# Kernel tuning notes

Hardware: AMD Instinct MI355X
Metric: run time of the kernel (lower is better)

The kernel has to match this reference:

```python
import jax, jax.numpy as jnp
import numpy as np

DIM_MSA = 256
DIM_PAIR = 128
DIM_HID = 32
EPS = 0.001
LN_EPS = 1e-5


def setup_inputs() -> dict:
    key = jax.random.key(0)
    ks = jax.random.split(key, 8)
    b, m, n = 1, 256, 384
    x = jax.random.normal(ks[0], (b, m, n, DIM_MSA), dtype=jnp.float32)
    mask = jax.random.randint(ks[1], (b, m, n), 0, 2).astype(jnp.int32)
    ln_g = jnp.ones((DIM_MSA,), jnp.float32)
    ln_b = jnp.zeros((DIM_MSA,), jnp.float32)
    s = 1.0 / np.sqrt(DIM_MSA)
    wl = jax.random.normal(ks[2], (DIM_MSA, DIM_HID), jnp.float32) * s
    bl = jnp.zeros((DIM_HID,), jnp.float32)
    wr = jax.random.normal(ks[3], (DIM_MSA, DIM_HID), jnp.float32) * s
    br = jnp.zeros((DIM_HID,), jnp.float32)
    wo = jax.random.normal(ks[4], (DIM_HID * DIM_HID, DIM_PAIR), jnp.float32) / np.sqrt(DIM_HID * DIM_HID)
    bo = jnp.zeros((DIM_PAIR,), jnp.float32)
    return {"x": x, "mask": mask, "ln_g": ln_g, "ln_b": ln_b,
            "wl": wl, "bl": bl, "wr": wr, "br": br, "wo": wo, "bo": bo}


def reference(x, mask, ln_g, ln_b, wl, bl, wr, br, wo, bo):
    # LayerNorm over last dim
    mu = jnp.mean(x, axis=-1, keepdims=True)
    var = jnp.mean(jnp.square(x - mu), axis=-1, keepdims=True)
    xn = (x - mu) * jax.lax.rsqrt(var + LN_EPS) * ln_g + ln_b
    left = xn @ wl + bl    # [b,m,n,c]
    right = xn @ wr + br   # [b,m,n,d]
    m = mask.astype(x.dtype)  # 0/1 mask [b,m,n]
    left = left * m[..., None]
    right = right * m[..., None]
    # masked outer-product sum over MSA dim m, no 6D materialization
    outer = jnp.einsum('bmic,bmjd->bijcd', left, right)
    b_, i_, j_ = outer.shape[0], outer.shape[1], outer.shape[2]
    outer = outer.reshape(b_, i_, j_, DIM_HID * DIM_HID)
    out = outer @ wo + bo  # [b,i,j,pairwise]
    cnt = jnp.einsum('bmi,bmj->bij', m, m)  # valid-pair counts
    return out / (cnt[..., None] + EPS)
```

## Files before the change

### kernel.cpp

```cpp
#include <hip/hip_runtime.h>
#include <hip/hip_bf16.h>
#include <stdint.h>


typedef float f32x4 __attribute__((ext_vector_type(4)));
typedef __bf16 bf16x8 __attribute__((ext_vector_type(8)));

#define NSEQ 384
#define NMSA 256

typedef const __attribute__((address_space(1))) unsigned int* gptr_t;
typedef __attribute__((address_space(3))) unsigned int* lptr_t;

__device__ __forceinline__ void gload_lds16(const void* g, void* l) {
    __builtin_amdgcn_global_load_lds((gptr_t)g, (lptr_t)l, 16, 0, 0);
}

__global__ __launch_bounds__(256) void prep_kernel(
    const float* __restrict__ wl, const float* __restrict__ wr,
    const float* __restrict__ bl, const float* __restrict__ br,
    const float* __restrict__ wo,
    __bf16* __restrict__ woT, __bf16* __restrict__ wT, float* __restrict__ bias2)
{
    int gid = blockIdx.x * 256 + threadIdx.x;
    if (gid < 131072) {
        int p = gid >> 10, k = gid & 1023;
        woT[gid] = (__bf16)wo[k * 128 + p];
    } else if (gid < 131072 + 16384) {
        int r = gid - 131072;
        int c = r >> 8, k = r & 255;
        wT[r] = (__bf16)(c < 32 ? wl[k * 32 + c] : wr[k * 32 + (c - 32)]);
    } else if (gid < 131072 + 16384 + 64) {
        int c = gid - 147456;
        bias2[c] = (c < 32) ? bl[c] : br[c - 32];
    }
}

__global__ __launch_bounds__(256) void cnt_kernel(
    const int* __restrict__ mask, float* __restrict__ inv_cnt)
{
    const int i = blockIdx.x;
    const int t = threadIdx.x;
    __shared__ int mi[NMSA];
    mi[t] = mask[t * NSEQ + i];
    __syncthreads();
    for (int j = t; j < NSEQ; j += 256) {
        int acc = 0;
        for (int m = 0; m < NMSA; ++m)
            acc += mi[m] & mask[m * NSEQ + j];
        inv_cnt[i * NSEQ + j] = 1.0f / ((float)acc + 0.001f);
    }
}

__global__ __launch_bounds__(256) void ln_proj_kernel(
    const float* __restrict__ x, const int* __restrict__ mask,
    const float* __restrict__ ln_g, const float* __restrict__ ln_b,
    const __bf16* __restrict__ wT, const float* __restrict__ bias2,
    __bf16* __restrict__ leftT, __bf16* __restrict__ rightT)
{
    const int n = blockIdx.x;
    const int tid = threadIdx.x;
    __shared__ float muS[NMSA], rsS[NMSA], maskS[NMSA];
    __shared__ __bf16 xnT[NMSA * 40];

    {
        const float* xr = x + ((size_t)tid * NSEQ + n) * 256;
        float s = 0.f, sq = 0.f;
        for (int k = 0; k < 256; k += 4) {
            f32x4 v = *reinterpret_cast<const f32x4*>(xr + k);
            s  += v[0] + v[1] + v[2] + v[3];
            sq += v[0]*v[0] + v[1]*v[1] + v[2]*v[2] + v[3]*v[3];
        }
        float mu = s * (1.f / 256.f);
        float var = sq * (1.f / 256.f) - mu * mu;
        muS[tid] = mu;
        rsS[tid] = rsqrtf(var + 1e-5f);
        maskS[tid] = (float)mask[tid * NSEQ + n];
    }
    __syncthreads();

    const int wid = tid >> 6, lane = tid & 63;
    const int lhi = lane >> 4, llo = lane & 15;
    f32x4 acc[4][4] = {};

    for (int k0 = 0; k0 < 256; k0 += 32) {
        #pragma unroll
        for (int cc = 0; cc < 8; ++cc) {
            int ch = tid + cc * 256;
            int mR = ch >> 3, c4 = ch & 7;
            f32x4 v  = *reinterpret_cast<const f32x4*>(x + ((size_t)mR * NSEQ + n) * 256 + k0 + c4 * 4);
            f32x4 g  = *reinterpret_cast<const f32x4*>(ln_g + k0 + c4 * 4);
            f32x4 bb = *reinterpret_cast<const f32x4*>(ln_b + k0 + c4 * 4);
            float mu = muS[mR], rs = rsS[mR];
            __bf16* dst = xnT + mR * 40 + c4 * 4;
            dst[0] = (__bf16)((v[0] - mu) * rs * g[0] + bb[0]);
            dst[1] = (__bf16)((v[1] - mu) * rs * g[1] + bb[1]);
            dst[2] = (__bf16)((v[2] - mu) * rs * g[2] + bb[2]);
            dst[3] = (__bf16)((v[3] - mu) * rs * g[3] + bb[3]);
        }
        __syncthreads();
        bf16x8 af[4], bfr[4];
        #pragma unroll
        for (int fr = 0; fr < 4; ++fr)
            af[fr] = *reinterpret_cast<const bf16x8*>(wT + (size_t)(fr * 16 + llo) * 256 + k0 + lhi * 8);
        #pragma unroll
        for (int fc = 0; fc < 4; ++fc)
            bfr[fc] = *reinterpret_cast<const bf16x8*>(xnT + (wid * 64 + fc * 16 + llo) * 40 + lhi * 8);
        #pragma unroll
        for (int fr = 0; fr < 4; ++fr)
            #pragma unroll
            for (int fc = 0; fc < 4; ++fc)
                acc[fr][fc] = __builtin_amdgcn_mfma_f32_16x16x32_bf16(af[fr], bfr[fc], acc[fr][fc], 0, 0, 0);
        __syncthreads();
    }

    #pragma unroll
    for (int fr = 0; fr < 4; ++fr) {
        #pragma unroll
        for (int fc = 0; fc < 4; ++fc) {
            int mR = wid * 64 + fc * 16 + llo;
            float mv = maskS[mR];
            #pragma unroll
            for (int r = 0; r < 4; ++r) {
                int c = fr * 16 + lhi * 4 + r;
                __bf16 bv = (__bf16)((acc[fr][fc][r] + bias2[c]) * mv);
                if (c < 32) leftT [(size_t)(n * 32 + c)        * 256 + mR] = bv;
                else        rightT[(size_t)(n * 32 + (c - 32)) * 256 + mR] = bv;
            }
        }
    }
}

__global__ __launch_bounds__(512, 2) void outer_gemm_kernel(
    const __bf16* __restrict__ leftT, const __bf16* __restrict__ rightT,
    const __bf16* __restrict__ woT, const float* __restrict__ bo,
    const float* __restrict__ inv_cnt, float* __restrict__ out)
{
    __shared__ char smem[131072];
    const int tid = threadIdx.x;
    const int wid = tid >> 6, lane = tid & 63;
    const int lhi = lane >> 4, llo = lane & 15;
    const int wr = wid >> 2, wc = wid & 3;

    int wg = blockIdx.x;
    int l  = (wg & 7) * 288 + (wg >> 3);
    int bj = l / 48, bi = l % 48;

    char* Abuf[2] = { smem,         smem + 65536 };
    char* Bbuf[2] = { smem + 32768, smem + 98304 };

    auto STAGE = [&](int buf, int k0) {
        #pragma unroll
        for (int it = 0; it < 4; ++it) {
            int q = it * 512 + wid * 64 + lane;
            int r = q >> 3;
            int s = (q & 7) ^ (r & 7);
            int ldsoff = (it * 512 + wid * 64) * 16;
            gload_lds16(leftT  + (size_t)(bi * 256 + r) * 256 + k0 + s * 8, Abuf[buf] + ldsoff);
            gload_lds16(rightT + (size_t)(bj * 256 + r) * 256 + k0 + s * 8, Bbuf[buf] + ldsoff);
        }
    };

    f32x4 acc[8][4] = {};

    STAGE(0, 0);
    #pragma unroll
    for (int t = 0; t < 4; ++t) {
        if (t < 3) {
            STAGE((t + 1) & 1, (t + 1) * 64);
            asm volatile("s_waitcnt vmcnt(8)" ::: "memory");
        } else {
            asm volatile("s_waitcnt vmcnt(0)" ::: "memory");
        }
        __builtin_amdgcn_s_barrier();
        __builtin_amdgcn_sched_barrier(0);
        const __bf16* Al = (const __bf16*)Abuf[t & 1];
        const __bf16* Bl = (const __bf16*)Bbuf[t & 1];
        #pragma unroll
        for (int kk = 0; kk < 2; ++kk) {
            bf16x8 af[8], bfv[4];
            int sb = kk * 4 + lhi;
            #pragma unroll
            for (int fr = 0; fr < 8; ++fr) {
                int row = wr * 128 + fr * 16 + llo;
                af[fr] = *(const bf16x8*)(Al + row * 64 + ((sb ^ (row & 7)) << 3));
            }
            #pragma unroll
            for (int fc = 0; fc < 4; ++fc) {
                int row = wc * 64 + fc * 16 + llo;
                bfv[fc] = *(const bf16x8*)(Bl + row * 64 + ((sb ^ (row & 7)) << 3));
            }
            #pragma unroll
            for (int fr = 0; fr < 8; ++fr)
                #pragma unroll
                for (int fc = 0; fc < 4; ++fc)
                    acc[fr][fc] = __builtin_amdgcn_mfma_f32_16x16x32_bf16(af[fr], bfv[fc], acc[fr][fc], 0, 0, 0);
        }
        __builtin_amdgcn_sched_barrier(0);
        __builtin_amdgcn_s_barrier();
    }

    __bf16* Aep = (__bf16*)smem;
    #pragma unroll
    for (int fr = 0; fr < 8; ++fr) {
        #pragma unroll
        for (int fc = 0; fc < 4; ++fc) {
            int gj = wc * 64 + fc * 16 + llo;
            int jl = gj >> 5, d = gj & 31;
            #pragma unroll
            for (int r = 0; r < 4; ++r) {
                int gi = wr * 128 + fr * 16 + lhi * 4 + r;
                int il = gi >> 5, c = gi & 31;
                int ij = il * 8 + jl;
                int cd = c * 32 + d;
                int s = cd >> 3;
                int ss = s ^ ((s >> 4) & 7) ^ (ij & 7);
                Aep[ij * 1024 + (ss << 3) + (cd & 7)] = (__bf16)acc[fr][fc][r];
            }
        }
    }
    __builtin_amdgcn_s_barrier();
    __builtin_amdgcn_sched_barrier(0);

    f32x4 eacc[4] = {};
    const int p = wid * 16 + llo;
    const __bf16* wrow = woT + (size_t)p * 1024 + lhi * 8;
    #pragma unroll 4
    for (int k0 = 0; k0 < 1024; k0 += 32) {
        int sb = (k0 >> 3) + lhi;
        bf16x8 bw = *(const bf16x8*)(wrow + k0);
        #pragma unroll
        for (int mf = 0; mf < 4; ++mf) {
            int ij = mf * 16 + llo;
            int ss = sb ^ ((sb >> 4) & 7) ^ (ij & 7);
            bf16x8 a = *(const bf16x8*)(Aep + ij * 1024 + (ss << 3));
            eacc[mf] = __builtin_amdgcn_mfma_f32_16x16x32_bf16(a, bw, eacc[mf], 0, 0, 0);
        }
    }

    const float bov = bo[p];
    #pragma unroll
    for (int mf = 0; mf < 4; ++mf) {
        #pragma unroll
        for (int r = 0; r < 4; ++r) {
            int ij = mf * 16 + lhi * 4 + r;
            int i = bi * 8 + (ij >> 3);
            int j = bj * 8 + (ij & 7);
            size_t idx = (size_t)i * NSEQ + j;
            out[idx * 128 + p] = (eacc[mf][r] + bov) * inv_cnt[idx];
        }
    }
}

extern "C" void kernel_launch(void* const* d_in, const int* in_sizes, int n_in,
                              void* d_out, int out_size, void* d_ws, size_t ws_size,
                              hipStream_t stream) {
    const float* x    = (const float*)d_in[0];
    const int*   mask = (const int*)  d_in[1];
    const float* ln_g = (const float*)d_in[2];
    const float* ln_b = (const float*)d_in[3];
    const float* wl   = (const float*)d_in[4];
    const float* bl   = (const float*)d_in[5];
    const float* wr   = (const float*)d_in[6];
    const float* br   = (const float*)d_in[7];
    const float* wo   = (const float*)d_in[8];
    const float* bo   = (const float*)d_in[9];
    float* out = (float*)d_out;

    char* ws = (char*)d_ws;
    __bf16* leftT   = (__bf16*)(ws);
    __bf16* rightT  = (__bf16*)(ws + 6291456);
    __bf16* woT     = (__bf16*)(ws + 12582912);
    __bf16* wT      = (__bf16*)(ws + 12845056);
    float*  bias2   = (float*) (ws + 12877824);
    float*  inv_cnt = (float*) (ws + 12878080);

    prep_kernel<<<577, 256, 0, stream>>>(wl, wr, bl, br, wo, woT, wT, bias2);
    cnt_kernel<<<NSEQ, 256, 0, stream>>>(mask, inv_cnt);
    ln_proj_kernel<<<NSEQ, 256, 0, stream>>>(x, mask, ln_g, ln_b, wT, bias2, leftT, rightT);
    outer_gemm_kernel<<<2304, 512, 0, stream>>>(leftT, rightT, woT, bo, inv_cnt, out);
}
```

Measured before the change: 220.1 us.

## Fold LayerNorm into projection weights and split epilogue K across waves

LayerNorm gamma/beta are folded into the projection weights, with per-column sums precomputed. The projection kernel therefore reads x once, feeding raw bf16 x to the MFMA while accumulating row statistics, and applies mean/rstd correction in the epilogue. This removes the separate pass over x for statistics. In the outer GEMM epilogue, the accumulator write-out uses vectorized bf16x4 stores with a permuted woT layout, and the 1024-long K reduction is split across two wave groups combined through LDS. Rounding raw x to bf16 before subtracting the mean may cost some accuracy.

```diff
diff --git a/kernel.cpp b/kernel.cpp
--- a/kernel.cpp
+++ b/kernel.cpp
@@ -5,6 +5,7 @@
 
 typedef float f32x4 __attribute__((ext_vector_type(4)));
 typedef __bf16 bf16x8 __attribute__((ext_vector_type(8)));
+typedef __bf16 bf16x4 __attribute__((ext_vector_type(4)));
 
 #define NSEQ 384
 #define NMSA 256
@@ -17,22 +18,38 @@
 }
 
 __global__ __launch_bounds__(256) void prep_kernel(
+    const float* __restrict__ wo, __bf16* __restrict__ woT)
+{
+    int gid = blockIdx.x * 256 + threadIdx.x;
+    int p = gid >> 10, q = gid & 1023;
+    int d = q >> 5, c = q & 31;
+    woT[gid] = (__bf16)wo[(c * 32 + d) * 128 + p];
+}
+
+__global__ __launch_bounds__(256) void prep_wg_kernel(
     const float* __restrict__ wl, const float* __restrict__ wr,
     const float* __restrict__ bl, const float* __restrict__ br,
-    const float* __restrict__ wo,
-    __bf16* __restrict__ woT, __bf16* __restrict__ wT, float* __restrict__ bias2)
-{
-    int gid = blockIdx.x * 256 + threadIdx.x;
-    if (gid < 131072) {
-        int p = gid >> 10, k = gid & 1023;
-        woT[gid] = (__bf16)wo[k * 128 + p];
-    } else if (gid < 131072 + 16384) {
-        int r = gid - 131072;
-        int c = r >> 8, k = r & 255;
-        wT[r] = (__bf16)(c < 32 ? wl[k * 32 + c] : wr[k * 32 + (c - 32)]);
-    } else if (gid < 131072 + 16384 + 64) {
-        int c = gid - 147456;
-        bias2[c] = (c < 32) ? bl[c] : br[c - 32];
+    const float* __restrict__ ln_g, const float* __restrict__ ln_b,
+    __bf16* __restrict__ wg, float* __restrict__ Gc, float* __restrict__ B2)
+{
+    const int c = blockIdx.x;
+    const int k = threadIdx.x;
+    float w = (c < 32) ? wl[k * 32 + c] : wr[k * 32 + (c - 32)];
+    __bf16 wgb = (__bf16)(w * ln_g[k]);
+    wg[c * 256 + k] = wgb;
+    float gsum = (float)wgb;
+    float bsum = w * ln_b[k];
+    __shared__ float sg[4], sb[4];
+    for (int off = 32; off; off >>= 1) {
+        gsum += __shfl_down(gsum, off);
+        bsum += __shfl_down(bsum, off);
+    }
+    int wid = k >> 6, lane = k & 63;
+    if (lane == 0) { sg[wid] = gsum; sb[wid] = bsum; }
+    __syncthreads();
+    if (k == 0) {
+        Gc[c] = sg[0] + sg[1] + sg[2] + sg[3];
+        B2[c] = sb[0] + sb[1] + sb[2] + sb[3] + ((c < 32) ? bl[c] : br[c - 32]);
     }
 }
 
@@ -54,33 +71,21 @@
 
 __global__ __launch_bounds__(256) void ln_proj_kernel(
     const float* __restrict__ x, const int* __restrict__ mask,
-    const float* __restrict__ ln_g, const float* __restrict__ ln_b,
-    const __bf16* __restrict__ wT, const float* __restrict__ bias2,
+    const __bf16* __restrict__ wg, const float* __restrict__ Gc,
+    const float* __restrict__ B2,
     __bf16* __restrict__ leftT, __bf16* __restrict__ rightT)
 {
     const int n = blockIdx.x;
     const int tid = threadIdx.x;
-    __shared__ float muS[NMSA], rsS[NMSA], maskS[NMSA];
     __shared__ __bf16 xnT[NMSA * 40];
-
-    {
-        const float* xr = x + ((size_t)tid * NSEQ + n) * 256;
-        float s = 0.f, sq = 0.f;
-        for (int k = 0; k < 256; k += 4) {
-            f32x4 v = *reinterpret_cast<const f32x4*>(xr + k);
-            s  += v[0] + v[1] + v[2] + v[3];
-            sq += v[0]*v[0] + v[1]*v[1] + v[2]*v[2] + v[3]*v[3];
-        }
-        float mu = s * (1.f / 256.f);
-        float var = sq * (1.f / 256.f) - mu * mu;
-        muS[tid] = mu;
-        rsS[tid] = rsqrtf(var + 1e-5f);
-        maskS[tid] = (float)mask[tid * NSEQ + n];
-    }
-    __syncthreads();
+    __shared__ float muS[NMSA], rsS[NMSA], maskS[NMSA], GcS[64], B2S[64];
+
+    if (tid < 64) { GcS[tid] = Gc[tid]; B2S[tid] = B2[tid]; }
+    maskS[tid] = (float)mask[tid * NSEQ + n];
 
     const int wid = tid >> 6, lane = tid & 63;
     const int lhi = lane >> 4, llo = lane & 15;
+    float ps[8] = {}, pq[8] = {};
     f32x4 acc[4][4] = {};
 
     for (int k0 = 0; k0 < 256; k0 += 32) {
@@ -88,21 +93,18 @@
         for (int cc = 0; cc < 8; ++cc) {
             int ch = tid + cc * 256;
             int mR = ch >> 3, c4 = ch & 7;
-            f32x4 v  = *reinterpret_cast<const f32x4*>(x + ((size_t)mR * NSEQ + n) * 256 + k0 + c4 * 4);
-            f32x4 g  = *reinterpret_cast<const f32x4*>(ln_g + k0 + c4 * 4);
-            f32x4 bb = *reinterpret_cast<const f32x4*>(ln_b + k0 + c4 * 4);
-            float mu = muS[mR], rs = rsS[mR];
+            f32x4 v = *reinterpret_cast<const f32x4*>(x + ((size_t)mR * NSEQ + n) * 256 + k0 + c4 * 4);
+            ps[cc] += v[0] + v[1] + v[2] + v[3];
+            pq[cc] += v[0]*v[0] + v[1]*v[1] + v[2]*v[2] + v[3]*v[3];
             __bf16* dst = xnT + mR * 40 + c4 * 4;
-            dst[0] = (__bf16)((v[0] - mu) * rs * g[0] + bb[0]);
-            dst[1] = (__bf16)((v[1] - mu) * rs * g[1] + bb[1]);
-            dst[2] = (__bf16)((v[2] - mu) * rs * g[2] + bb[2]);
-            dst[3] = (__bf16)((v[3] - mu) * rs * g[3] + bb[3]);
+            dst[0] = (__bf16)v[0]; dst[1] = (__bf16)v[1];
+            dst[2] = (__bf16)v[2]; dst[3] = (__bf16)v[3];
         }
         __syncthreads();
         bf16x8 af[4], bfr[4];
         #pragma unroll
         for (int fr = 0; fr < 4; ++fr)
-            af[fr] = *reinterpret_cast<const bf16x8*>(wT + (size_t)(fr * 16 + llo) * 256 + k0 + lhi * 8);
+            af[fr] = *reinterpret_cast<const bf16x8*>(wg + (size_t)(fr * 16 + llo) * 256 + k0 + lhi * 8);
         #pragma unroll
         for (int fc = 0; fc < 4; ++fc)
             bfr[fc] = *reinterpret_cast<const bf16x8*>(xnT + (wid * 64 + fc * 16 + llo) * 40 + lhi * 8);
@@ -115,15 +117,32 @@
     }
 
     #pragma unroll
+    for (int cc = 0; cc < 8; ++cc) {
+        float s = ps[cc], q = pq[cc];
+        s += __shfl_xor(s, 1); q += __shfl_xor(q, 1);
+        s += __shfl_xor(s, 2); q += __shfl_xor(q, 2);
+        s += __shfl_xor(s, 4); q += __shfl_xor(q, 4);
+        if ((tid & 7) == 0) {
+            int m = (tid >> 3) + cc * 32;
+            float mu = s * (1.f / 256.f);
+            float var = q * (1.f / 256.f) - mu * mu;
+            muS[m] = mu;
+            rsS[m] = rsqrtf(var + 1e-5f);
+        }
+    }
+    __syncthreads();
+
+    #pragma unroll
     for (int fr = 0; fr < 4; ++fr) {
         #pragma unroll
         for (int fc = 0; fc < 4; ++fc) {
             int mR = wid * 64 + fc * 16 + llo;
-            float mv = maskS[mR];
+            float mv = maskS[mR], rs = rsS[mR], mu = muS[mR];
             #pragma unroll
             for (int r = 0; r < 4; ++r) {
                 int c = fr * 16 + lhi * 4 + r;
-                __bf16 bv = (__bf16)((acc[fr][fc][r] + bias2[c]) * mv);
+                float val = (acc[fr][fc][r] - mu * GcS[c]) * rs + B2S[c];
+                __bf16 bv = (__bf16)(val * mv);
                 if (c < 32) leftT [(size_t)(n * 32 + c)        * 256 + mR] = bv;
                 else        rightT[(size_t)(n * 32 + (c - 32)) * 256 + mR] = bv;
             }
@@ -142,8 +161,8 @@
     const int lhi = lane >> 4, llo = lane & 15;
     const int wr = wid >> 2, wc = wid & 3;
 
-    int wg = blockIdx.x;
-    int l  = (wg & 7) * 288 + (wg >> 3);
+    int wg_ = blockIdx.x;
+    int l  = (wg_ & 7) * 288 + (wg_ >> 3);
     int bj = l / 48, bi = l % 48;
 
     char* Abuf[2] = { smem,         smem + 65536 };
@@ -205,50 +224,66 @@
     for (int fr = 0; fr < 8; ++fr) {
         #pragma unroll
         for (int fc = 0; fc < 4; ++fc) {
-            int gj = wc * 64 + fc * 16 + llo;
-            int jl = gj >> 5, d = gj & 31;
-            #pragma unroll
-            for (int r = 0; r < 4; ++r) {
-                int gi = wr * 128 + fr * 16 + lhi * 4 + r;
-                int il = gi >> 5, c = gi & 31;
-                int ij = il * 8 + jl;
-                int cd = c * 32 + d;
-                int s = cd >> 3;
-                int ss = s ^ ((s >> 4) & 7) ^ (ij & 7);
-                Aep[ij * 1024 + (ss << 3) + (cd & 7)] = (__bf16)acc[fr][fc][r];
-            }
-        }
-    }
-    __builtin_amdgcn_s_barrier();
-    __builtin_amdgcn_sched_barrier(0);
-
-    f32x4 eacc[4] = {};
-    const int p = wid * 16 + llo;
-    const __bf16* wrow = woT + (size_t)p * 1024 + lhi * 8;
-    #pragma unroll 4
-    for (int k0 = 0; k0 < 1024; k0 += 32) {
-        int sb = (k0 >> 3) + lhi;
-        bf16x8 bw = *(const bf16x8*)(wrow + k0);
+            int ij = (wr * 4 + (fr >> 1)) * 8 + wc * 2 + (fc >> 1);
+            int half = fc & 1;
+            int t = llo * 4 + (fr & 1) * 2 + (lhi >> 1);
+            int tp = t ^ ((t >> 3) & 7) ^ (ij & 7);
+            bf16x4 v;
+            v[0] = (__bf16)acc[fr][fc][0]; v[1] = (__bf16)acc[fr][fc][1];
+            v[2] = (__bf16)acc[fr][fc][2]; v[3] = (__bf16)acc[fr][fc][3];
+            *(bf16x4*)(Aep + half * 32768 + ij * 512 + tp * 8 + (lhi & 1) * 4) = v;
+        }
+    }
+    __syncthreads();
+
+    const int kw = wid & 1, nw = wid >> 1;
+    const __bf16* Asrc = Aep + kw * 32768;
+    f32x4 eacc[4][2] = {};
+    #pragma unroll 2
+    for (int k0 = 0; k0 < 512; k0 += 32) {
+        bf16x8 bw0 = *(const bf16x8*)(woT + (size_t)(nw * 32 + llo)      * 1024 + kw * 512 + k0 + lhi * 8);
+        bf16x8 bw1 = *(const bf16x8*)(woT + (size_t)(nw * 32 + 16 + llo) * 1024 + kw * 512 + k0 + lhi * 8);
+        int t = (k0 >> 3) + lhi;
+        int txor = (t >> 3) & 7;
         #pragma unroll
         for (int mf = 0; mf < 4; ++mf) {
             int ij = mf * 16 + llo;
-            int ss = sb ^ ((sb >> 4) & 7) ^ (ij & 7);
-            bf16x8 a = *(const bf16x8*)(Aep + ij * 1024 + (ss << 3));
-            eacc[mf] = __builtin_amdgcn_mfma_f32_16x16x32_bf16(a, bw, eacc[mf], 0, 0, 0);
-        }
-    }
-
-    const float bov = bo[p];
-    #pragma unroll
-    for (int mf = 0; mf < 4; ++mf) {
-        #pragma unroll
-        for (int r = 0; r < 4; ++r) {
-            int ij = mf * 16 + lhi * 4 + r;
-            int i = bi * 8 + (ij >> 3);
-            int j = bj * 8 + (ij & 7);
-            size_t idx = (size_t)i * NSEQ + j;
-            out[idx * 128 + p] = (eacc[mf][r] + bov) * inv_cnt[idx];
-        }
+            int tp = t ^ txor ^ (ij & 7);
+            bf16x8 a = *(const bf16x8*)(Asrc + ij * 512 + tp * 8);
+            eacc[mf][0] = __builtin_amdgcn_mfma_f32_16x16x32_bf16(a, bw0, eacc[mf][0], 0, 0, 0);
+            eacc[mf][1] = __builtin_amdgcn_mfma_f32_16x16x32_bf16(a, bw1, eacc[mf][1], 0, 0, 0);
+        }
+    }
+    __syncthreads();
+
+    float* scratch = (float*)smem;
+    if (kw == 1) {
+        #pragma unroll
+        for (int mf = 0; mf < 4; ++mf)
+            #pragma unroll
+            for (int pf = 0; pf < 2; ++pf) {
+                int p = nw * 32 + pf * 16 + llo;
+                #pragma unroll
+                for (int r = 0; r < 4; ++r)
+                    scratch[(mf * 16 + lhi * 4 + r) * 132 + p] = eacc[mf][pf][r];
+            }
+    }
+    __syncthreads();
+    if (kw == 0) {
+        #pragma unroll
+        for (int mf = 0; mf < 4; ++mf)
+            #pragma unroll
+            for (int pf = 0; pf < 2; ++pf) {
+                int p = nw * 32 + pf * 16 + llo;
+                float bov = bo[p];
+                #pragma unroll
+                for (int r = 0; r < 4; ++r) {
+                    int ij = mf * 16 + lhi * 4 + r;
+                    int i = bi * 8 + (ij >> 3), j = bj * 8 + (ij & 7);
+                    size_t idx = (size_t)i * NSEQ + j;
+                    out[idx * 128 + p] = (eacc[mf][pf][r] + scratch[ij * 132 + p] + bov) * inv_cnt[idx];
+                }
+            }
     }
 }
 
@@ -271,12 +306,14 @@
     __bf16* leftT   = (__bf16*)(ws);
     __bf16* rightT  = (__bf16*)(ws + 6291456);
     __bf16* woT     = (__bf16*)(ws + 12582912);
-    __bf16* wT      = (__bf16*)(ws + 12845056);
-    float*  bias2   = (float*) (ws + 12877824);
-    float*  inv_cnt = (float*) (ws + 12878080);
-
-    prep_kernel<<<577, 256, 0, stream>>>(wl, wr, bl, br, wo, woT, wT, bias2);
+    __bf16* wg      = (__bf16*)(ws + 12845056);
+    float*  Gc      = (float*) (ws + 12877824);
+    float*  B2      = (float*) (ws + 12878080);
+    float*  inv_cnt = (float*) (ws + 12878336);
+
+    prep_kernel<<<512, 256, 0, stream>>>(wo, woT);
+    prep_wg_kernel<<<64, 256, 0, stream>>>(wl, wr, bl, br, ln_g, ln_b, wg, Gc, B2);
     cnt_kernel<<<NSEQ, 256, 0, stream>>>(mask, inv_cnt);
-    ln_proj_kernel<<<NSEQ, 256, 0, stream>>>(x, mask, ln_g, ln_b, wT, bias2, leftT, rightT);
+    ln_proj_kernel<<<NSEQ, 256, 0, stream>>>(x, mask, wg, Gc, B2, leftT, rightT);
     outer_gemm_kernel<<<2304, 512, 0, stream>>>(leftT, rightT, woT, bo, inv_cnt, out);
 }
```

Result: no change. 218.6 us (-0.7%).
